# Kernel optimization log

Hardware: AMD Instinct MI355X
Metric: run time of the kernel (lower is better)

## Reference

```python
import jax, jax.numpy as jnp
import numpy as np

B, T, I, H, O = 128, 4096, 6, 32, 2


def setup_inputs() -> dict:
    key = jax.random.key(0)
    ks = jax.random.split(key, 8)
    x = jax.random.normal(ks[0], (B, T, I), dtype=jnp.float32)
    lengths = jax.random.randint(ks[1], (B,), 1, T + 1, dtype=jnp.int32)
    lengths = jnp.sort(lengths)[::-1]            # descending (enforce_sorted=True)
    lengths = lengths.at[0].set(T)               # max length == T -> static output shape
    s = 1.0 / np.sqrt(H)                         # PyTorch GRU/Linear init scale
    w_ih = jax.random.uniform(ks[2], (3 * H, I), minval=-s, maxval=s, dtype=jnp.float32)
    w_hh = jax.random.uniform(ks[3], (3 * H, H), minval=-s, maxval=s, dtype=jnp.float32)
    b_ih = jax.random.uniform(ks[4], (3 * H,), minval=-s, maxval=s, dtype=jnp.float32)
    b_hh = jax.random.uniform(ks[5], (3 * H,), minval=-s, maxval=s, dtype=jnp.float32)
    fc_w = jax.random.uniform(ks[6], (O, H), minval=-s, maxval=s, dtype=jnp.float32)
    fc_b = jax.random.uniform(ks[7], (O,), minval=-s, maxval=s, dtype=jnp.float32)
    return {"x": x, "lengths": lengths, "w_ih": w_ih, "w_hh": w_hh,
            "b_ih": b_ih, "b_hh": b_hh, "fc_w": fc_w, "fc_b": fc_b}


def reference(x, lengths, w_ih, w_hh, b_ih, b_hh, fc_w, fc_b):
    Bn, Tn, _ = x.shape
    Hn = w_hh.shape[1]
    # Precompute input-side gate projections for all steps (one big GEMM).
    gx = jnp.einsum('bti,gi->btg', x, w_ih) + b_ih      # [B,T,3H] (gate order: r,z,n)
    gx = jnp.swapaxes(gx, 0, 1)                          # [T,B,3H] time-major for scan
    mask = jnp.arange(Tn)[:, None] < lengths[None, :]    # [T,B] valid-step mask
    h0 = jnp.zeros((Bn, Hn), x.dtype)

    def step(h, inp):
        gxt, m = inp                                     # gxt [B,3H], m [B]
        gh = h @ w_hh.T + b_hh                           # [B,3H]
        xr, xz, xn = jnp.split(gxt, 3, axis=-1)
        hr, hz, hn = jnp.split(gh, 3, axis=-1)
        r = jax.nn.sigmoid(xr + hr)
        z = jax.nn.sigmoid(xz + hz)
        n = jnp.tanh(xn + r * hn)
        h_new = (1.0 - z) * n + z * h
        m = m[:, None]
        out = jnp.where(m, h_new, 0.0)                   # pad_packed pads with zeros
        h = jnp.where(m, h_new, h)                       # freeze state past length
        return h, out

    _, ys = jax.lax.scan(step, h0, (gx, mask))           # ys [T,B,H]
    out = jnp.swapaxes(ys, 0, 1)                         # [B,T,H]
    # fc applied to every (incl. zero-padded) timestep, as in the torch code
    return jnp.einsum('bth,oh->bto', out, fc_w) + fc_b   # [B,T,O]
```

## Files before the change

kernel.cpp:

```cpp
#include <hip/hip_runtime.h>

#define TT 4096
#define BB 128
#define L2E 1.4426950408889634f

typedef unsigned uv2 __attribute__((ext_vector_type(2)));
typedef float v2f __attribute__((ext_vector_type(2)));
typedef float v4f __attribute__((ext_vector_type(4)));
typedef __bf16 v8bf __attribute__((ext_vector_type(8)));

__device__ __forceinline__ float fexp2(float a) { return __builtin_amdgcn_exp2f(a); }

__device__ __forceinline__ float bpermf(int idx_bytes, float v) {
  return __int_as_float(__builtin_amdgcn_ds_bpermute(idx_bytes, __float_as_int(v)));
}

__device__ __forceinline__ float xhalf_sum(float p) {
#if __has_builtin(__builtin_amdgcn_permlane32_swap)
  uv2 r = __builtin_amdgcn_permlane32_swap(__float_as_uint(p), __float_as_uint(p),
                                           false, false);
  return __uint_as_float(r[0]) + __uint_as_float(r[1]);
#else
  return p + bpermf((threadIdx.x ^ 32) << 2, p);
#endif
}

__device__ __forceinline__ unsigned cvtpk(float lo, float hi) {
  unsigned r;
  asm("v_cvt_pk_bf16_f32 %0, %1, %2" : "=v"(r) : "v"(lo), "v"(hi));
  return r;
}

__device__ __forceinline__ v8bf frag_from(unsigned u0, unsigned u1, unsigned u2,
                                          unsigned u3) {
  uint4 uu = make_uint4(u0, u1, u2, u3);
  return __builtin_bit_cast(v8bf, uu);
}

__global__ __launch_bounds__(256) void gx_pre(
    const float* __restrict__ x, const float* __restrict__ w_ih,
    const float* __restrict__ b_ih, const float* __restrict__ b_hh,
    const int* __restrict__ lengths, float* __restrict__ gx) {
  const size_t idx = (size_t)blockIdx.x * 256 + threadIdx.x;
  const int g = (int)(idx % 96);
  const size_t bt = idx / 96;
  const int b = (int)(bt >> 12);
  const int t = (int)(bt & (TT - 1));
  if (t >= lengths[b]) return;
  const float* xp = x + bt * 6;
  float acc = (g < 64) ? (b_ih[g] + b_hh[g]) : b_ih[g];
#pragma unroll
  for (int i = 0; i < 6; ++i) acc = fmaf(w_ih[g * 6 + i], xp[i], acc);
  gx[idx] = (g < 64) ? (L2E * acc) : (2.0f * L2E * acc);
}

__global__ __launch_bounds__(64) __attribute__((amdgpu_waves_per_eu(1, 1)))
void gru_seq(const int* __restrict__ lengths, const float* __restrict__ w_hh,
             const float* __restrict__ b_hh, const float* __restrict__ gx,
             float* __restrict__ hbuf) {
  __shared__ alignas(16) float hring[2][32][32];

  const int b = blockIdx.x;
  const int l = threadIdx.x;
  const int j = l & 31;
  const int len = lengths[b];
  const int n_ = l & 15;
  const int kb = (l >> 4) * 8;

  auto make_wfrag = [&](int grow, int jb, float scale) -> v8bf {
    const float* wrow = w_hh + (grow + jb + n_) * 32 + kb;
    unsigned u0 = cvtpk(wrow[0] * scale, wrow[1] * scale);
    unsigned u1 = cvtpk(wrow[2] * scale, wrow[3] * scale);
    unsigned u2 = cvtpk(wrow[4] * scale, wrow[5] * scale);
    unsigned u3 = cvtpk(wrow[6] * scale, wrow[7] * scale);
    return frag_from(u0, u1, u2, u3);
  };
  const v8bf fR0 = make_wfrag(0, 0, L2E),          fR1 = make_wfrag(0, 16, L2E);
  const v8bf fZ0 = make_wfrag(32, 0, L2E),         fZ1 = make_wfrag(32, 16, L2E);
  const v8bf fN0 = make_wfrag(64, 0, 2.0f * L2E),  fN1 = make_wfrag(64, 16, 2.0f * L2E);
  v4f cn0, cn1;
  {
    const float c0 = 2.0f * L2E * b_hh[64 + n_];
    const float c1 = 2.0f * L2E * b_hh[80 + n_];
    cn0 = v4f{c0, c0, c0, c0};
    cn1 = v4f{c1, c1, c1, c1};
  }
  const v4f zero4 = v4f{0.f, 0.f, 0.f, 0.f};
  const bool hiSel = ((l >> 4) & 1);

  const float* gxb = gx + (size_t)b * TT * 96;
  float* hrow = hbuf + (size_t)b * TT * 32;
  const int bpbase = (l >> 4) << 5;

  float h = 0.0f;
  int t = 0;

  float g0r, g0z, g0n, g1r, g1z, g1n, g2r, g2z, g2n, g3r, g3z, g3n;
  {
    const int t1 = (1 < len) ? 1 : len - 1, t2 = (2 < len) ? 2 : len - 1,
              t3 = (3 < len) ? 3 : len - 1;
    const float *p0 = gxb, *p1 = gxb + (size_t)t1 * 96,
                *p2 = gxb + (size_t)t2 * 96, *p3 = gxb + (size_t)t3 * 96;
    g0r = p0[j]; g0z = p0[32 + j]; g0n = p0[64 + j];
    g1r = p1[j]; g1z = p1[32 + j]; g1n = p1[64 + j];
    g2r = p2[j]; g2z = p2[32 + j]; g2n = p2[64 + j];
    g3r = p3[j]; g3z = p3[32 + j]; g3n = p3[64 + j];
  }

  auto flush = [&](int base, int cnt) {
    const float4* src = (const float4*)(&hring[(base >> 5) & 1][0][0]);
    float4* dst = (float4*)(hrow + (size_t)base * 32);
    const int n4 = cnt * 8;
    for (int q = l; q < n4; q += 64) dst[q] = src[q];
  };

  auto step = [&](float& GR, float& GZ, float& GN) {
    const float xr_ = GR, xz_ = GZ, xn_ = GN;
    {
      const int tp = (t + 4 < len) ? (t + 4) : (len - 1);
      const float* gp = gxb + (size_t)tp * 96;
      GR = gp[j]; GZ = gp[32 + j]; GN = gp[64 + j];
    }

    const float p0 = bpermf(bpbase + 0, h),  p1 = bpermf(bpbase + 4, h);
    const float p2 = bpermf(bpbase + 8, h),  p3 = bpermf(bpbase + 12, h);
    const float p4 = bpermf(bpbase + 16, h), p5 = bpermf(bpbase + 20, h);
    const float p6 = bpermf(bpbase + 24, h), p7 = bpermf(bpbase + 28, h);
    const v8bf ha = frag_from(cvtpk(p0, p1), cvtpk(p2, p3),
                              cvtpk(p4, p5), cvtpk(p6, p7));

    const v4f yr0 = __builtin_amdgcn_mfma_f32_16x16x32_bf16(ha, fR0, zero4, 0, 0, 0);
    const v4f yr1 = __builtin_amdgcn_mfma_f32_16x16x32_bf16(ha, fR1, zero4, 0, 0, 0);
    const v4f yz0 = __builtin_amdgcn_mfma_f32_16x16x32_bf16(ha, fZ0, zero4, 0, 0, 0);
    const v4f yz1 = __builtin_amdgcn_mfma_f32_16x16x32_bf16(ha, fZ1, zero4, 0, 0, 0);
    const v4f yn0 = __builtin_amdgcn_mfma_f32_16x16x32_bf16(ha, fN0, cn0, 0, 0, 0);
    const v4f yn1 = __builtin_amdgcn_mfma_f32_16x16x32_bf16(ha, fN1, cn1, 0, 0, 0);

    const float yr = hiSel ? yr1[0] : yr0[0];
    const float yz = hiSel ? yz1[0] : yz0[0];
    const float hn = hiSel ? yn1[0] : yn0[0];

    const float r_ = __builtin_amdgcn_rcpf(1.0f + fexp2(-(yr + xr_)));
    const float z_ = __builtin_amdgcn_rcpf(1.0f + fexp2(-(yz + xz_)));
    const float ap = fmaf(r_, hn, xn_);
    const float q_ = __builtin_amdgcn_rcpf(1.0f + fexp2(-ap));
    const float nn = fmaf(2.0f, q_, -1.0f);
    h = fmaf(z_, h - nn, nn);

    hring[(t >> 5) & 1][t & 31][j] = h;
    if ((t & 31) == 31) flush(t - 31, 32);
    ++t;
  };

  while (t + 4 <= len) {
    step(g0r, g0z, g0n);
    step(g1r, g1z, g1n);
    step(g2r, g2z, g2n);
    step(g3r, g3z, g3n);
  }
  if (t < len) step(g0r, g0z, g0n);
  if (t < len) step(g1r, g1z, g1n);
  if (t < len) step(g2r, g2z, g2n);

  const int rem = len & 31;
  if (rem) flush(len - rem, rem);
}

__global__ __launch_bounds__(256) void fc_apply(
    const float* __restrict__ hbuf, const int* __restrict__ lengths,
    const float* __restrict__ fc_w, const float* __restrict__ fc_b,
    float* __restrict__ out) {
  const int idx = blockIdx.x * 256 + threadIdx.x;
  const int b = idx >> 12;
  const int t = idx & (TT - 1);
  const float fb0 = fc_b[0], fb1 = fc_b[1];
  float* op = out + (size_t)idx * 2;
  if (t >= lengths[b]) {
    op[0] = fb0;
    op[1] = fb1;
    return;
  }
  const float4* hp = (const float4*)(hbuf + (size_t)idx * 32);
  const float4* w0 = (const float4*)(fc_w);
  const float4* w1 = (const float4*)(fc_w + 32);
  float o0 = 0.f, o1 = 0.f;
#pragma unroll
  for (int q = 0; q < 8; ++q) {
    const float4 hv = hp[q], a = w0[q], c = w1[q];
    o0 += hv.x * a.x + hv.y * a.y + hv.z * a.z + hv.w * a.w;
    o1 += hv.x * c.x + hv.y * c.y + hv.z * c.z + hv.w * c.w;
  }
  op[0] = o0 + fb0;
  op[1] = o1 + fb1;
}

__global__ __launch_bounds__(64) void gru_fallback(
    const float* __restrict__ x, const int* __restrict__ lengths,
    const float* __restrict__ w_ih, const float* __restrict__ w_hh,
    const float* __restrict__ b_ih, const float* __restrict__ b_hh,
    const float* __restrict__ fc_w, const float* __restrict__ fc_b,
    float* __restrict__ out) {
  const int b = blockIdx.x;
  const int l = threadIdx.x;
  const int j = l & 31;
  const int half = l >> 5;
  const int ko = half << 4;
  const int len = lengths[b];

  float wr[16], wz[16], wn[16];
#pragma unroll
  for (int k = 0; k < 16; ++k) wr[k] = w_hh[j * 32 + ko + k] * L2E;
#pragma unroll
  for (int k = 0; k < 16; ++k) wz[k] = w_hh[(32 + j) * 32 + ko + k] * L2E;
#pragma unroll
  for (int k = 0; k < 16; ++k) wn[k] = w_hh[(64 + j) * 32 + ko + k] * (2.0f * L2E);
  float wxr[6], wxz[6], wxn[6];
#pragma unroll
  for (int i = 0; i < 6; ++i) wxr[i] = w_ih[j * 6 + i] * (0.5f * L2E);
#pragma unroll
  for (int i = 0; i < 6; ++i) wxz[i] = w_ih[(32 + j) * 6 + i] * (0.5f * L2E);
#pragma unroll
  for (int i = 0; i < 6; ++i) wxn[i] = w_ih[(64 + j) * 6 + i] * (2.0f * L2E);
  const float br = (b_ih[j] + b_hh[j]) * (0.5f * L2E);
  const float bz = (b_ih[32 + j] + b_hh[32 + j]) * (0.5f * L2E);
  const float bxn = b_ih[64 + j] * (2.0f * L2E);
  const float bhn = b_hh[64 + j] * L2E;
  const float fcw = fc_w[half * 32 + j];
  const float fcb = fc_b[half];

  const float* xb = x + (size_t)b * (TT * 6);
  float* ob = out + (size_t)b * (TT * 2);
  const int bko = half << 6;
  float h = 0.0f;

  v2f cx[3], nx[3];
  {
    const v2f* xp = (const v2f*)xb;
    cx[0] = xp[0]; cx[1] = xp[1]; cx[2] = xp[2];
  }
  for (int t = 0; t < len; ++t) {
    const int tn = (t + 1 < len) ? (t + 1) : t;
    const v2f* xp = (const v2f*)(xb + tn * 6);
    nx[0] = xp[0]; nx[1] = xp[1]; nx[2] = xp[2];
    float xr = br, xz = bz, xn = bxn;
#pragma unroll
    for (int i = 0; i < 3; ++i) {
      const float c0 = cx[i][0], c1 = cx[i][1];
      xr = fmaf(wxr[2 * i], c0, xr); xr = fmaf(wxr[2 * i + 1], c1, xr);
      xz = fmaf(wxz[2 * i], c0, xz); xz = fmaf(wxz[2 * i + 1], c1, xz);
      xn = fmaf(wxn[2 * i], c0, xn); xn = fmaf(wxn[2 * i + 1], c1, xn);
    }
    float hbv[16];
#pragma unroll
    for (int k = 0; k < 16; ++k) hbv[k] = bpermf(bko + (k << 2), h);
    float ar0 = xr, ar1 = 0.f, az0 = xz, az1 = 0.f, an0 = bhn, an1 = 0.f;
#pragma unroll
    for (int k = 0; k < 8; ++k) {
      ar0 = fmaf(wr[k], hbv[k], ar0);
      ar1 = fmaf(wr[k + 8], hbv[k + 8], ar1);
      az0 = fmaf(wz[k], hbv[k], az0);
      az1 = fmaf(wz[k + 8], hbv[k + 8], az1);
      an0 = fmaf(wn[k], hbv[k], an0);
      an1 = fmaf(wn[k + 8], hbv[k + 8], an1);
    }
    const float sr = xhalf_sum(ar0 + ar1);
    const float r = __builtin_amdgcn_rcpf(1.0f + fexp2(-sr));
    const float sz = xhalf_sum(az0 + az1);
    const float z = __builtin_amdgcn_rcpf(1.0f + fexp2(-sz));
    const float hn = xhalf_sum(an0 + an1);
    const float ap = fmaf(r, hn, xn);
    const float qq = __builtin_amdgcn_rcpf(1.0f + fexp2(-ap));
    const float nn = fmaf(2.0f, qq, -1.0f);
    h = fmaf(z, h - nn, nn);
    float p = h * fcw;
    p += __shfl_xor(p, 1);
    p += __shfl_xor(p, 2);
    p += __shfl_xor(p, 4);
    p += __shfl_xor(p, 8);
    p += __shfl_xor(p, 16);
    if (j == 0) ob[t * 2 + half] = p + fcb;
#pragma unroll
    for (int i = 0; i < 3; ++i) cx[i] = nx[i];
  }
  const float fb0 = fc_b[0], fb1 = fc_b[1];
  for (int idx = len * 2 + l; idx < TT * 2; idx += 64)
    ob[idx] = (idx & 1) ? fb1 : fb0;
}

extern "C" void kernel_launch(void* const* d_in, const int* in_sizes, int n_in,
                              void* d_out, int out_size, void* d_ws, size_t ws_size,
                              hipStream_t stream) {
  const float* x       = (const float*)d_in[0];
  const int*   lengths = (const int*)d_in[1];
  const float* w_ih    = (const float*)d_in[2];
  const float* w_hh    = (const float*)d_in[3];
  const float* b_ih    = (const float*)d_in[4];
  const float* b_hh    = (const float*)d_in[5];
  const float* fc_w    = (const float*)d_in[6];
  const float* fc_b    = (const float*)d_in[7];
  float* outp = (float*)d_out;

  const size_t hbuf_elems = (size_t)BB * TT * 32;
  const size_t gx_elems   = (size_t)BB * TT * 96;
  const size_t need = (hbuf_elems + gx_elems) * sizeof(float);
  if (ws_size >= need) {
    float* hbuf = (float*)d_ws;
    float* gx = (float*)d_ws + hbuf_elems;
    hipLaunchKernelGGL(gx_pre, dim3((BB * TT * 96) / 256), dim3(256), 0, stream,
                       x, w_ih, b_ih, b_hh, lengths, gx);
    hipLaunchKernelGGL(gru_seq, dim3(BB), dim3(64), 0, stream,
                       lengths, w_hh, b_hh, gx, hbuf);
    hipLaunchKernelGGL(fc_apply, dim3((BB * TT) / 256), dim3(256), 0, stream,
                       hbuf, lengths, fc_w, fc_b, outp);
  } else {
    hipLaunchKernelGGL(gru_fallback, dim3(BB), dim3(64), 0, stream,
                       x, lengths, w_ih, w_hh, b_ih, b_hh, fc_w, fc_b, outp);
  }
}
```

Baseline: 863.2 us.

## Swap MFMA operand roles so hidden state feeds back via DPP instead of bpermute

Makes the weight matrix the A operand and the hidden state the B operand of the per-step MFMAs. Rows are permuted so each lane owns two hidden units whose results land in registers it can use directly. The eight ds_bpermute broadcasts per step are replaced by one bf16 pack plus four DPP quad-broadcasts, taking LDS round trips off the serial recurrence path. In exchange each lane now evaluates two gate sets per step, adding ALU and transcendental work and more select logic.

New measurement: 1.032 ms. 19.5% more time.

```diff
diff --git a/kernel.cpp b/kernel.cpp
--- a/kernel.cpp
+++ b/kernel.cpp
@@ -62,105 +62,133 @@
 
   const int b = blockIdx.x;
   const int l = threadIdx.x;
-  const int j = l & 31;
+  const int g = l >> 4;
+  const int n_ = l & 15;
+  const int q = n_ & 3;
+  const int kb = g * 8;
+  const int row0 = kb + 2 * q;
   const int len = lengths[b];
-  const int n_ = l & 15;
-  const int kb = (l >> 4) * 8;
-
-  auto make_wfrag = [&](int grow, int jb, float scale) -> v8bf {
-    const float* wrow = w_hh + (grow + jb + n_) * 32 + kb;
+
+  auto make_wfragA = [&](int grow, int plus4, float scale) -> v8bf {
+    const int prow = 8 * (n_ >> 2) + (n_ & 3) + plus4;
+    const float* wrow = w_hh + (grow + prow) * 32 + kb;
     unsigned u0 = cvtpk(wrow[0] * scale, wrow[1] * scale);
     unsigned u1 = cvtpk(wrow[2] * scale, wrow[3] * scale);
     unsigned u2 = cvtpk(wrow[4] * scale, wrow[5] * scale);
     unsigned u3 = cvtpk(wrow[6] * scale, wrow[7] * scale);
     return frag_from(u0, u1, u2, u3);
   };
-  const v8bf fR0 = make_wfrag(0, 0, L2E),          fR1 = make_wfrag(0, 16, L2E);
-  const v8bf fZ0 = make_wfrag(32, 0, L2E),         fZ1 = make_wfrag(32, 16, L2E);
-  const v8bf fN0 = make_wfrag(64, 0, 2.0f * L2E),  fN1 = make_wfrag(64, 16, 2.0f * L2E);
-  v4f cn0, cn1;
-  {
-    const float c0 = 2.0f * L2E * b_hh[64 + n_];
-    const float c1 = 2.0f * L2E * b_hh[80 + n_];
-    cn0 = v4f{c0, c0, c0, c0};
-    cn1 = v4f{c1, c1, c1, c1};
+  const v8bf fRa = make_wfragA(0, 0, L2E),  fRb = make_wfragA(0, 4, L2E);
+  const v8bf fZa = make_wfragA(32, 0, L2E), fZb = make_wfragA(32, 4, L2E);
+  const v8bf fNa = make_wfragA(64, 0, 2.0f * L2E), fNb = make_wfragA(64, 4, 2.0f * L2E);
+  v4f cna, cnb;
+#pragma unroll
+  for (int i = 0; i < 4; ++i) {
+    cna[i] = 2.0f * L2E * b_hh[64 + kb + i];
+    cnb[i] = 2.0f * L2E * b_hh[64 + kb + 4 + i];
   }
   const v4f zero4 = v4f{0.f, 0.f, 0.f, 0.f};
-  const bool hiSel = ((l >> 4) & 1);
+  const bool c1 = (q & 1) != 0;
+  const bool c2 = (q & 2) != 0;
 
   const float* gxb = gx + (size_t)b * TT * 96;
   float* hrow = hbuf + (size_t)b * TT * 32;
-  const int bpbase = (l >> 4) << 5;
-
-  float h = 0.0f;
+
+  float h0 = 0.f, h1 = 0.f;
+  v8bf hb = frag_from(0u, 0u, 0u, 0u);
+
   int t = 0;
 
-  float g0r, g0z, g0n, g1r, g1z, g1n, g2r, g2z, g2n, g3r, g3z, g3n;
+  float s0a, s0b, s0c, s0d, s0e, s0f;
+  float s1a, s1b, s1c, s1d, s1e, s1f;
+  float s2a, s2b, s2c, s2d, s2e, s2f;
+  float s3a, s3b, s3c, s3d, s3e, s3f;
   {
     const int t1 = (1 < len) ? 1 : len - 1, t2 = (2 < len) ? 2 : len - 1,
               t3 = (3 < len) ? 3 : len - 1;
     const float *p0 = gxb, *p1 = gxb + (size_t)t1 * 96,
                 *p2 = gxb + (size_t)t2 * 96, *p3 = gxb + (size_t)t3 * 96;
-    g0r = p0[j]; g0z = p0[32 + j]; g0n = p0[64 + j];
-    g1r = p1[j]; g1z = p1[32 + j]; g1n = p1[64 + j];
-    g2r = p2[j]; g2z = p2[32 + j]; g2n = p2[64 + j];
-    g3r = p3[j]; g3z = p3[32 + j]; g3n = p3[64 + j];
+    s0a = p0[row0]; s0b = p0[row0 + 1]; s0c = p0[32 + row0]; s0d = p0[33 + row0];
+    s0e = p0[64 + row0]; s0f = p0[65 + row0];
+    s1a = p1[row0]; s1b = p1[row0 + 1]; s1c = p1[32 + row0]; s1d = p1[33 + row0];
+    s1e = p1[64 + row0]; s1f = p1[65 + row0];
+    s2a = p2[row0]; s2b = p2[row0 + 1]; s2c = p2[32 + row0]; s2d = p2[33 + row0];
+    s2e = p2[64 + row0]; s2f = p2[65 + row0];
+    s3a = p3[row0]; s3b = p3[row0 + 1]; s3c = p3[32 + row0]; s3d = p3[33 + row0];
+    s3e = p3[64 + row0]; s3f = p3[65 + row0];
   }
 
   auto flush = [&](int base, int cnt) {
     const float4* src = (const float4*)(&hring[(base >> 5) & 1][0][0]);
     float4* dst = (float4*)(hrow + (size_t)base * 32);
     const int n4 = cnt * 8;
-    for (int q = l; q < n4; q += 64) dst[q] = src[q];
+    for (int qq = l; qq < n4; qq += 64) dst[qq] = src[qq];
   };
 
-  auto step = [&](float& GR, float& GZ, float& GN) {
-    const float xr_ = GR, xz_ = GZ, xn_ = GN;
+  auto sel2 = [&](v4f fa, v4f fb, float& y0, float& y1) {
+    const float a0 = c1 ? fa[2] : fa[0], a1 = c1 ? fa[3] : fa[1];
+    const float b0 = c1 ? fb[2] : fb[0], b1 = c1 ? fb[3] : fb[1];
+    y0 = c2 ? b0 : a0;
+    y1 = c2 ? b1 : a1;
+  };
+
+  auto step = [&](float& XR0, float& XR1, float& XZ0, float& XZ1, float& XN0,
+                  float& XN1) {
+    const float xr0 = XR0, xr1 = XR1, xz0 = XZ0, xz1 = XZ1, xn0 = XN0, xn1 = XN1;
     {
       const int tp = (t + 4 < len) ? (t + 4) : (len - 1);
       const float* gp = gxb + (size_t)tp * 96;
-      GR = gp[j]; GZ = gp[32 + j]; GN = gp[64 + j];
+      XR0 = gp[row0]; XR1 = gp[row0 + 1];
+      XZ0 = gp[32 + row0]; XZ1 = gp[33 + row0];
+      XN0 = gp[64 + row0]; XN1 = gp[65 + row0];
     }
 
-    const float p0 = bpermf(bpbase + 0, h),  p1 = bpermf(bpbase + 4, h);
-    const float p2 = bpermf(bpbase + 8, h),  p3 = bpermf(bpbase + 12, h);
-    const float p4 = bpermf(bpbase + 16, h), p5 = bpermf(bpbase + 20, h);
-    const float p6 = bpermf(bpbase + 24, h), p7 = bpermf(bpbase + 28, h);
-    const v8bf ha = frag_from(cvtpk(p0, p1), cvtpk(p2, p3),
-                              cvtpk(p4, p5), cvtpk(p6, p7));
-
-    const v4f yr0 = __builtin_amdgcn_mfma_f32_16x16x32_bf16(ha, fR0, zero4, 0, 0, 0);
-    const v4f yr1 = __builtin_amdgcn_mfma_f32_16x16x32_bf16(ha, fR1, zero4, 0, 0, 0);
-    const v4f yz0 = __builtin_amdgcn_mfma_f32_16x16x32_bf16(ha, fZ0, zero4, 0, 0, 0);
-    const v4f yz1 = __builtin_amdgcn_mfma_f32_16x16x32_bf16(ha, fZ1, zero4, 0, 0, 0);
-    const v4f yn0 = __builtin_amdgcn_mfma_f32_16x16x32_bf16(ha, fN0, cn0, 0, 0, 0);
-    const v4f yn1 = __builtin_amdgcn_mfma_f32_16x16x32_bf16(ha, fN1, cn1, 0, 0, 0);
-
-    const float yr = hiSel ? yr1[0] : yr0[0];
-    const float yz = hiSel ? yz1[0] : yz0[0];
-    const float hn = hiSel ? yn1[0] : yn0[0];
-
-    const float r_ = __builtin_amdgcn_rcpf(1.0f + fexp2(-(yr + xr_)));
-    const float z_ = __builtin_amdgcn_rcpf(1.0f + fexp2(-(yz + xz_)));
-    const float ap = fmaf(r_, hn, xn_);
-    const float q_ = __builtin_amdgcn_rcpf(1.0f + fexp2(-ap));
-    const float nn = fmaf(2.0f, q_, -1.0f);
-    h = fmaf(z_, h - nn, nn);
-
-    hring[(t >> 5) & 1][t & 31][j] = h;
+    const v4f yra = __builtin_amdgcn_mfma_f32_16x16x32_bf16(fRa, hb, zero4, 0, 0, 0);
+    const v4f yrb = __builtin_amdgcn_mfma_f32_16x16x32_bf16(fRb, hb, zero4, 0, 0, 0);
+    const v4f yza = __builtin_amdgcn_mfma_f32_16x16x32_bf16(fZa, hb, zero4, 0, 0, 0);
+    const v4f yzb = __builtin_amdgcn_mfma_f32_16x16x32_bf16(fZb, hb, zero4, 0, 0, 0);
+    const v4f yna = __builtin_amdgcn_mfma_f32_16x16x32_bf16(fNa, hb, cna, 0, 0, 0);
+    const v4f ynb = __builtin_amdgcn_mfma_f32_16x16x32_bf16(fNb, hb, cnb, 0, 0, 0);
+
+    float yr0, yr1, yz0, yz1, hn0, hn1;
+    sel2(yra, yrb, yr0, yr1);
+    sel2(yza, yzb, yz0, yz1);
+    sel2(yna, ynb, hn0, hn1);
+
+    const float r0 = __builtin_amdgcn_rcpf(1.0f + fexp2(-(yr0 + xr0)));
+    const float r1 = __builtin_amdgcn_rcpf(1.0f + fexp2(-(yr1 + xr1)));
+    const float z0 = __builtin_amdgcn_rcpf(1.0f + fexp2(-(yz0 + xz0)));
+    const float z1 = __builtin_amdgcn_rcpf(1.0f + fexp2(-(yz1 + xz1)));
+    const float ap0 = fmaf(r0, hn0, xn0);
+    const float ap1 = fmaf(r1, hn1, xn1);
+    const float q0 = __builtin_amdgcn_rcpf(1.0f + fexp2(-ap0));
+    const float q1 = __builtin_amdgcn_rcpf(1.0f + fexp2(-ap1));
+    const float nn0 = fmaf(2.0f, q0, -1.0f);
+    const float nn1 = fmaf(2.0f, q1, -1.0f);
+    h0 = fmaf(z0, h0 - nn0, nn0);
+    h1 = fmaf(z1, h1 - nn1, nn1);
+
+    const int dw = (int)cvtpk(h0, h1);
+    const int u0 = __builtin_amdgcn_update_dpp(0, dw, 0x00, 0xF, 0xF, true);
+    const int u1 = __builtin_amdgcn_update_dpp(0, dw, 0x55, 0xF, 0xF, true);
+    const int u2 = __builtin_amdgcn_update_dpp(0, dw, 0xAA, 0xF, 0xF, true);
+    const int u3 = __builtin_amdgcn_update_dpp(0, dw, 0xFF, 0xF, 0xF, true);
+    hb = frag_from((unsigned)u0, (unsigned)u1, (unsigned)u2, (unsigned)u3);
+
+    *(float2*)(&hring[(t >> 5) & 1][t & 31][row0]) = make_float2(h0, h1);
     if ((t & 31) == 31) flush(t - 31, 32);
     ++t;
   };
 
   while (t + 4 <= len) {
-    step(g0r, g0z, g0n);
-    step(g1r, g1z, g1n);
-    step(g2r, g2z, g2n);
-    step(g3r, g3z, g3n);
-  }
-  if (t < len) step(g0r, g0z, g0n);
-  if (t < len) step(g1r, g1z, g1n);
-  if (t < len) step(g2r, g2z, g2n);
+    step(s0a, s0b, s0c, s0d, s0e, s0f);
+    step(s1a, s1b, s1c, s1d, s1e, s1f);
+    step(s2a, s2b, s2c, s2d, s2e, s2f);
+    step(s3a, s3b, s3c, s3d, s3e, s3f);
+  }
+  if (t < len) step(s0a, s0b, s0c, s0d, s0e, s0f);
+  if (t < len) step(s1a, s1b, s1c, s1d, s1e, s1f);
+  if (t < len) step(s2a, s2b, s2c, s2d, s2e, s2f);
 
   const int rem = len & 31;
   if (rem) flush(len - rem, rem);
@@ -185,8 +213,8 @@
   const float4* w1 = (const float4*)(fc_w + 32);
   float o0 = 0.f, o1 = 0.f;
 #pragma unroll
-  for (int q = 0; q < 8; ++q) {
-    const float4 hv = hp[q], a = w0[q], c = w1[q];
+  for (int qq = 0; qq < 8; ++qq) {
+    const float4 hv = hp[qq], a = w0[qq], c = w1[qq];
     o0 += hv.x * a.x + hv.y * a.y + hv.z * a.z + hv.w * a.w;
     o1 += hv.x * c.x + hv.y * c.y + hv.z * c.z + hv.w * c.w;
   }
```
